# Optimization experiments

Measured on AMD Instinct MI355X. Metric: run time of the kernel, lower is better.

The kernel has to match this reference:

```python
import jax, jax.numpy as jnp
import numpy as np


def setup_inputs() -> dict:
    key = jax.random.key(0)
    k1, k2 = jax.random.split(key)
    B, N, M, D = 8, 4096, 4096, 128
    points1 = jax.random.normal(k1, (B, N, D), dtype=jnp.float32)
    points2 = jax.random.normal(k2, (B, M, D), dtype=jnp.float32)
    return {"points1": points1, "points2": points2}


def reference(points1, points2):
    # sum((x[:, :, None] - y[:, None, :])**2, -1), expressed as a GEMM).
    sq1 = jnp.sum(points1 * points1, axis=-1)              # [B, N]
    sq2 = jnp.sum(points2 * points2, axis=-1)              # [B, M]
    cross = jnp.einsum("bnd,bmd->bnm", points1, points2)   # [B, N, M]
    dist_matrix = sq1[:, :, None] + sq2[:, None, :] - 2.0 * cross
    min_dist1 = jnp.min(dist_matrix, axis=2)               # [B, N]
    min_dist2 = jnp.min(dist_matrix, axis=1)               # [B, M]
    return jnp.mean(min_dist1) + jnp.mean(min_dist2)
```

## Files before the change

kernel.cpp:

```cpp
#include <hip/hip_runtime.h>
#include <hip/hip_bf16.h>


#define BATCH 8
#define NPTS 4096
#define DIM 128

using bf16x8 = __attribute__((ext_vector_type(8))) short;
using f32x4  = __attribute__((ext_vector_type(4))) float;

__global__ void prep_kernel(const float* __restrict__ src,
                            __hip_bfloat16* __restrict__ dst,
                            float* __restrict__ sq) {
    const int wid = threadIdx.x >> 6;
    const int l   = threadIdx.x & 63;
    const int p   = blockIdx.x * 4 + wid;
    const float2 v = *reinterpret_cast<const float2*>(src + (size_t)p * DIM + l * 2);
    __hip_bfloat162 h = __float22bfloat162_rn(v);
    *reinterpret_cast<__hip_bfloat162*>(dst + (size_t)p * DIM + l * 2) = h;
    float s = v.x * v.x + v.y * v.y;
    #pragma unroll
    for (int off = 1; off < 64; off <<= 1) s += __shfl_xor(s, off);
    if (l == 0) sq[p] = s;
}

__global__ void __launch_bounds__(256, 2)
chamfer_tile_kernel(const __hip_bfloat16* __restrict__ bf1,
                    const __hip_bfloat16* __restrict__ bf2,
                    const float* __restrict__ sq1,
                    const float* __restrict__ sq2,
                    float* __restrict__ min1p,
                    float* __restrict__ min2p) {
    const int nt = blockIdx.x;
    const int mh = blockIdx.y;
    const int b  = blockIdx.z;
    const int tid = threadIdx.x;
    const int wid = tid >> 6;
    const int l   = tid & 63;
    const int l15 = l & 15;
    const int lhi = l >> 4;

    __shared__ __align__(16) unsigned char btile[128 * 256];
    __shared__ float colminbuf[4][128];
    __shared__ float sq2b[128];

    const __hip_bfloat16* bf1b = bf1 + (size_t)b * NPTS * DIM;
    const __hip_bfloat16* bf2b = bf2 + (size_t)b * NPTS * DIM;

    const int n0 = nt * 128 + wid * 32;

    bf16x8 afrag[2][4];
    #pragma unroll
    for (int rt = 0; rt < 2; ++rt)
        #pragma unroll
        for (int ks = 0; ks < 4; ++ks)
            afrag[rt][ks] = *reinterpret_cast<const bf16x8*>(
                bf1b + (n0 + rt * 16 + l15) * DIM + ks * 32 + lhi * 8);

    float sq1v[2][4];
    #pragma unroll
    for (int rt = 0; rt < 2; ++rt)
        #pragma unroll
        for (int j = 0; j < 4; ++j)
            sq1v[rt][j] = sq1[b * NPTS + n0 + rt * 16 + lhi * 4 + j];

    float rmin[2][4];
    #pragma unroll
    for (int rt = 0; rt < 2; ++rt)
        #pragma unroll
        for (int j = 0; j < 4; ++j) rmin[rt][j] = 3.4e38f;

    for (int mt = 0; mt < 16; ++mt) {
        const int m0 = mh * 2048 + mt * 128;

        __syncthreads();

        #pragma unroll
        for (int i = 0; i < 8; ++i) {
            const int c = i * 256 + tid;
            const int row = c >> 4;
            const int q   = c & 15;
            bf16x8 v = *reinterpret_cast<const bf16x8*>(
                bf2b + (m0 + row) * DIM + q * 8);
            const int dst = row * 256 + ((q * 16) ^ ((row & 7) << 4));
            *reinterpret_cast<bf16x8*>(&btile[dst]) = v;
        }
        if (tid < 128) sq2b[tid] = sq2[b * NPTS + m0 + tid];
        __syncthreads();

        f32x4 acc[2][8];
        #pragma unroll
        for (int rt = 0; rt < 2; ++rt)
            #pragma unroll
            for (int ct = 0; ct < 8; ++ct) acc[rt][ct] = f32x4{0.f, 0.f, 0.f, 0.f};

        #pragma unroll
        for (int ks = 0; ks < 4; ++ks) {
            #pragma unroll
            for (int ct = 0; ct < 8; ++ct) {
                const int brow = ct * 16 + l15;
                const int kbyte = ks * 64 + lhi * 16;
                bf16x8 bfrag = *reinterpret_cast<const bf16x8*>(
                    &btile[brow * 256 + (kbyte ^ ((brow & 7) << 4))]);
                #pragma unroll
                for (int rt = 0; rt < 2; ++rt)
                    acc[rt][ct] = __builtin_amdgcn_mfma_f32_16x16x32_bf16(
                        afrag[rt][ks], bfrag, acc[rt][ct], 0, 0, 0);
            }
        }

        float cmin[8];
        #pragma unroll
        for (int ct = 0; ct < 8; ++ct) cmin[ct] = 3.4e38f;

        #pragma unroll
        for (int rt = 0; rt < 2; ++rt) {
            #pragma unroll
            for (int ct = 0; ct < 8; ++ct) {
                const float s2 = sq2b[ct * 16 + l15];
                #pragma unroll
                for (int j = 0; j < 4; ++j) {
                    const float c2 = acc[rt][ct][j] + acc[rt][ct][j];
                    rmin[rt][j] = fminf(rmin[rt][j], s2 - c2);
                    cmin[ct]    = fminf(cmin[ct], sq1v[rt][j] - c2);
                }
            }
        }

        #pragma unroll
        for (int ct = 0; ct < 8; ++ct) {
            cmin[ct] = fminf(cmin[ct], __shfl_xor(cmin[ct], 16));
            cmin[ct] = fminf(cmin[ct], __shfl_xor(cmin[ct], 32));
        }
        if (l < 16) {
            #pragma unroll
            for (int ct = 0; ct < 8; ++ct) colminbuf[wid][ct * 16 + l] = cmin[ct];
        }
        __syncthreads();
        if (tid < 128) {
            float v = fminf(fminf(colminbuf[0][tid], colminbuf[1][tid]),
                            fminf(colminbuf[2][tid], colminbuf[3][tid]));
            min2p[((size_t)b * 32 + nt) * NPTS + m0 + tid] = v;
        }
    }

    #pragma unroll
    for (int rt = 0; rt < 2; ++rt)
        #pragma unroll
        for (int j = 0; j < 4; ++j) {
            float v = rmin[rt][j];
            v = fminf(v, __shfl_xor(v, 1));
            v = fminf(v, __shfl_xor(v, 2));
            v = fminf(v, __shfl_xor(v, 4));
            v = fminf(v, __shfl_xor(v, 8));
            rmin[rt][j] = v;
        }
    if (l15 == 0) {
        #pragma unroll
        for (int rt = 0; rt < 2; ++rt)
            #pragma unroll
            for (int j = 0; j < 4; ++j)
                min1p[((size_t)b * 2 + mh) * NPTS + n0 + rt * 16 + lhi * 4 + j] =
                    rmin[rt][j];
    }
}

__global__ void finalize_kernel(const float* __restrict__ min1p,
                                const float* __restrict__ min2p,
                                const float* __restrict__ sq1,
                                const float* __restrict__ sq2,
                                float* __restrict__ out) {
    const int tid = threadIdx.x;
    const int gid = blockIdx.x * 256 + tid;
    float sum = 0.f;

    for (int idx = gid; idx < BATCH * NPTS; idx += 64 * 256) {
        const int b = idx >> 12, n = idx & (NPTS - 1);
        const float v = fminf(min1p[(b * 2 + 0) * NPTS + n],
                              min1p[(b * 2 + 1) * NPTS + n]) + sq1[idx];
        sum += v;
    }
    for (int idx = gid; idx < BATCH * NPTS; idx += 64 * 256) {
        const int b = idx >> 12, m = idx & (NPTS - 1);
        float v = 3.4e38f;
        for (int nt = 0; nt < 32; ++nt)
            v = fminf(v, min2p[((size_t)b * 32 + nt) * NPTS + m]);
        sum += v + sq2[idx];
    }

    #pragma unroll
    for (int off = 1; off < 64; off <<= 1) sum += __shfl_xor(sum, off);
    __shared__ float wsum[4];
    if ((tid & 63) == 0) wsum[tid >> 6] = sum;
    __syncthreads();
    if (tid == 0) {
        const float t = wsum[0] + wsum[1] + wsum[2] + wsum[3];
        atomicAdd(out, t * (1.0f / (BATCH * NPTS)));
    }
}

extern "C" void kernel_launch(void* const* d_in, const int* in_sizes, int n_in,
                              void* d_out, int out_size, void* d_ws, size_t ws_size,
                              hipStream_t stream) {
    const float* p1 = (const float*)d_in[0];
    const float* p2 = (const float*)d_in[1];
    float* out = (float*)d_out;

    const size_t npts_tot = (size_t)BATCH * NPTS;
    __hip_bfloat16* bf1 = (__hip_bfloat16*)d_ws;
    __hip_bfloat16* bf2 = bf1 + npts_tot * DIM;
    float* sq1   = (float*)(bf2 + npts_tot * DIM);
    float* sq2   = sq1 + npts_tot;
    float* min1p = sq2 + npts_tot;
    float* min2p = min1p + (size_t)BATCH * 2 * NPTS;

    hipMemsetAsync(d_out, 0, sizeof(float), stream);

    prep_kernel<<<npts_tot / 4, 256, 0, stream>>>(p1, bf1, sq1);
    prep_kernel<<<npts_tot / 4, 256, 0, stream>>>(p2, bf2, sq2);

    dim3 g2(32, 2, BATCH);
    chamfer_tile_kernel<<<g2, 256, 0, stream>>>(bf1, bf2, sq1, sq2, min1p, min2p);

    finalize_kernel<<<64, 256, 0, stream>>>(min1p, min2p, sq1, sq2, out);
}
```

Measured before the change: 142.7 us.

## Fold -2 scale into bf16 prep, split M across more blocks, drop column-min sync

Folds the -2 factor into the bf16 conversion of points1 so the epilogue becomes plain add+min. It merges the two prep launches into one grid, doubles the M split (grid y 2->4) and raises the occupancy hint to 4 blocks per CU. It also removes the shared-memory column-min reduction and its extra __syncthreads, writing per-wave partials to global instead. The finalize kernel then gets one thread per output element and must reduce 128 partials per column, which adds partial-buffer traffic and workspace use.

Measured after the change: 209.7 us. +46.9%, slower.

```diff
diff --git a/kernel.cpp b/kernel.cpp
--- a/kernel.cpp
+++ b/kernel.cpp
@@ -9,22 +9,31 @@
 using bf16x8 = __attribute__((ext_vector_type(8))) short;
 using f32x4  = __attribute__((ext_vector_type(4))) float;
 
-__global__ void prep_kernel(const float* __restrict__ src,
-                            __hip_bfloat16* __restrict__ dst,
-                            float* __restrict__ sq) {
+__global__ void prep_kernel(const float* __restrict__ p1,
+                            const float* __restrict__ p2,
+                            __hip_bfloat16* __restrict__ b1,
+                            __hip_bfloat16* __restrict__ b2,
+                            float* __restrict__ s1,
+                            float* __restrict__ s2) {
+    const int arr = blockIdx.y;
+    const float* src = arr ? p2 : p1;
+    __hip_bfloat16* dst = arr ? b2 : b1;
+    float* sq = arr ? s2 : s1;
+    const float scale = arr ? 1.0f : -2.0f;
+
     const int wid = threadIdx.x >> 6;
     const int l   = threadIdx.x & 63;
     const int p   = blockIdx.x * 4 + wid;
     const float2 v = *reinterpret_cast<const float2*>(src + (size_t)p * DIM + l * 2);
-    __hip_bfloat162 h = __float22bfloat162_rn(v);
+    float s = v.x * v.x + v.y * v.y;
+    __hip_bfloat162 h = __float22bfloat162_rn(make_float2(v.x * scale, v.y * scale));
     *reinterpret_cast<__hip_bfloat162*>(dst + (size_t)p * DIM + l * 2) = h;
-    float s = v.x * v.x + v.y * v.y;
     #pragma unroll
     for (int off = 1; off < 64; off <<= 1) s += __shfl_xor(s, off);
     if (l == 0) sq[p] = s;
 }
 
-__global__ void __launch_bounds__(256, 2)
+__global__ void __launch_bounds__(256, 4)
 chamfer_tile_kernel(const __hip_bfloat16* __restrict__ bf1,
                     const __hip_bfloat16* __restrict__ bf2,
                     const float* __restrict__ sq1,
@@ -41,7 +50,6 @@
     const int lhi = l >> 4;
 
     __shared__ __align__(16) unsigned char btile[128 * 256];
-    __shared__ float colminbuf[4][128];
     __shared__ float sq2b[128];
 
     const __hip_bfloat16* bf1b = bf1 + (size_t)b * NPTS * DIM;
@@ -70,8 +78,8 @@
         #pragma unroll
         for (int j = 0; j < 4; ++j) rmin[rt][j] = 3.4e38f;
 
-    for (int mt = 0; mt < 16; ++mt) {
-        const int m0 = mh * 2048 + mt * 128;
+    for (int mt = 0; mt < 8; ++mt) {
+        const int m0 = mh * 1024 + mt * 128;
 
         __syncthreads();
 
@@ -109,22 +117,37 @@
             }
         }
 
+        float s2v[8];
+        #pragma unroll
+        for (int ct = 0; ct < 8; ++ct) s2v[ct] = sq2b[ct * 16 + l15];
+
+        #pragma unroll
+        for (int rt = 0; rt < 2; ++rt)
+            #pragma unroll
+            for (int j = 0; j < 4; ++j) {
+                float r = rmin[rt][j];
+                #pragma unroll
+                for (int cp = 0; cp < 4; ++cp) {
+                    const float t0 = acc[rt][2 * cp][j]     + s2v[2 * cp];
+                    const float t1 = acc[rt][2 * cp + 1][j] + s2v[2 * cp + 1];
+                    r = fminf(r, fminf(t0, t1));
+                }
+                rmin[rt][j] = r;
+            }
+
         float cmin[8];
         #pragma unroll
-        for (int ct = 0; ct < 8; ++ct) cmin[ct] = 3.4e38f;
-
-        #pragma unroll
-        for (int rt = 0; rt < 2; ++rt) {
-            #pragma unroll
-            for (int ct = 0; ct < 8; ++ct) {
-                const float s2 = sq2b[ct * 16 + l15];
+        for (int ct = 0; ct < 8; ++ct) {
+            float c = 3.4e38f;
+            #pragma unroll
+            for (int rt = 0; rt < 2; ++rt)
                 #pragma unroll
-                for (int j = 0; j < 4; ++j) {
-                    const float c2 = acc[rt][ct][j] + acc[rt][ct][j];
-                    rmin[rt][j] = fminf(rmin[rt][j], s2 - c2);
-                    cmin[ct]    = fminf(cmin[ct], sq1v[rt][j] - c2);
+                for (int jp = 0; jp < 2; ++jp) {
+                    const float u0 = sq1v[rt][2 * jp]     + acc[rt][ct][2 * jp];
+                    const float u1 = sq1v[rt][2 * jp + 1] + acc[rt][ct][2 * jp + 1];
+                    c = fminf(c, fminf(u0, u1));
                 }
-            }
+            cmin[ct] = c;
         }
 
         #pragma unroll
@@ -133,14 +156,9 @@
             cmin[ct] = fminf(cmin[ct], __shfl_xor(cmin[ct], 32));
         }
         if (l < 16) {
-            #pragma unroll
-            for (int ct = 0; ct < 8; ++ct) colminbuf[wid][ct * 16 + l] = cmin[ct];
-        }
-        __syncthreads();
-        if (tid < 128) {
-            float v = fminf(fminf(colminbuf[0][tid], colminbuf[1][tid]),
-                            fminf(colminbuf[2][tid], colminbuf[3][tid]));
-            min2p[((size_t)b * 32 + nt) * NPTS + m0 + tid] = v;
+            float* dst = min2p + ((size_t)b * 128 + nt * 4 + wid) * NPTS + m0;
+            #pragma unroll
+            for (int ct = 0; ct < 8; ++ct) dst[ct * 16 + l] = cmin[ct];
         }
     }
 
@@ -160,7 +178,7 @@
         for (int rt = 0; rt < 2; ++rt)
             #pragma unroll
             for (int j = 0; j < 4; ++j)
-                min1p[((size_t)b * 2 + mh) * NPTS + n0 + rt * 16 + lhi * 4 + j] =
+                min1p[((size_t)b * 4 + mh) * NPTS + n0 + rt * 16 + lhi * 4 + j] =
                     rmin[rt][j];
     }
 }
@@ -174,18 +192,22 @@
     const int gid = blockIdx.x * 256 + tid;
     float sum = 0.f;
 
-    for (int idx = gid; idx < BATCH * NPTS; idx += 64 * 256) {
-        const int b = idx >> 12, n = idx & (NPTS - 1);
-        const float v = fminf(min1p[(b * 2 + 0) * NPTS + n],
-                              min1p[(b * 2 + 1) * NPTS + n]) + sq1[idx];
-        sum += v;
-    }
-    for (int idx = gid; idx < BATCH * NPTS; idx += 64 * 256) {
+    if (gid < BATCH * NPTS) {
+        const int b = gid >> 12, n = gid & (NPTS - 1);
+        const float* p = min1p + (size_t)b * 4 * NPTS + n;
+        float v = fminf(fminf(p[0], p[NPTS]), fminf(p[2 * NPTS], p[3 * NPTS]));
+        sum = (v + sq1[gid]) * (1.0f / (BATCH * NPTS));
+    } else if (gid < 2 * BATCH * NPTS) {
+        const int idx = gid - BATCH * NPTS;
         const int b = idx >> 12, m = idx & (NPTS - 1);
-        float v = 3.4e38f;
-        for (int nt = 0; nt < 32; ++nt)
-            v = fminf(v, min2p[((size_t)b * 32 + nt) * NPTS + m]);
-        sum += v + sq2[idx];
+        const float* p = min2p + (size_t)b * 128 * NPTS + m;
+        float v0 = 3.4e38f, v1 = 3.4e38f;
+        #pragma unroll 4
+        for (int j = 0; j < 128; j += 2) {
+            v0 = fminf(v0, p[(size_t)j * NPTS]);
+            v1 = fminf(v1, p[(size_t)(j + 1) * NPTS]);
+        }
+        sum = (fminf(v0, v1) + sq2[idx]) * (1.0f / (BATCH * NPTS));
     }
 
     #pragma unroll
@@ -193,10 +215,7 @@
     __shared__ float wsum[4];
     if ((tid & 63) == 0) wsum[tid >> 6] = sum;
     __syncthreads();
-    if (tid == 0) {
-        const float t = wsum[0] + wsum[1] + wsum[2] + wsum[3];
-        atomicAdd(out, t * (1.0f / (BATCH * NPTS)));
-    }
+    if (tid == 0) atomicAdd(out, wsum[0] + wsum[1] + wsum[2] + wsum[3]);
 }
 
 extern "C" void kernel_launch(void* const* d_in, const int* in_sizes, int n_in,
@@ -212,15 +231,14 @@
     float* sq1   = (float*)(bf2 + npts_tot * DIM);
     float* sq2   = sq1 + npts_tot;
     float* min1p = sq2 + npts_tot;
-    float* min2p = min1p + (size_t)BATCH * 2 * NPTS;
+    float* min2p = min1p + (size_t)BATCH * 4 * NPTS;
 
     hipMemsetAsync(d_out, 0, sizeof(float), stream);
 
-    prep_kernel<<<npts_tot / 4, 256, 0, stream>>>(p1, bf1, sq1);
-    prep_kernel<<<npts_tot / 4, 256, 0, stream>>>(p2, bf2, sq2);
-
-    dim3 g2(32, 2, BATCH);
+    prep_kernel<<<dim3(npts_tot / 4, 2), 256, 0, stream>>>(p1, p2, bf1, bf2, sq1, sq2);
+
+    dim3 g2(32, 4, BATCH);
     chamfer_tile_kernel<<<g2, 256, 0, stream>>>(bf1, bf2, sq1, sq2, min1p, min2p);
 
-    finalize_kernel<<<64, 256, 0, stream>>>(min1p, min2p, sq1, sq2, out);
-}
+    finalize_kernel<<<512, 256, 0, stream>>>(min1p, min2p, sq1, sq2, out);
+}
```
